# Optimization experiments

Measured on AMD Instinct MI355X. Metric: run time of the kernel, lower is better.

## Reference

```python
import jax, jax.numpy as jnp
import numpy as np

# Complete 32-ary tree of depth 3: vocab = 32**3 = 32768 leaves.
B = 4096       # batch
NHID = 512     # hidden size
BR = 32        # branching factor (num_children at every internal node)
DEPTH = 3      # number of internal-node decisions from root to leaf
V = BR ** DEPTH
NUM_NODES = sum(BR ** k for k in range(DEPTH))  # 1 + 32 + 1024 = 1057

# Static tree-indexing tables (level-order node numbering).
_LEVEL_OFFSET = np.array([sum(BR ** j for j in range(k)) for k in range(DEPTH)], dtype=np.int64)   # [0, 1, 33]
_NODE_DIV = np.array([BR ** (DEPTH - k) for k in range(DEPTH)], dtype=np.int64)                    # node-within-level divisor
_STEP_DIV = np.array([BR ** (DEPTH - 1 - k) for k in range(DEPTH)], dtype=np.int64)                # child-step divisor


def setup_inputs() -> dict:
    key = jax.random.key(0)
    k1, k2, k3 = jax.random.split(key, 3)
    inputs = jax.random.normal(k1, (B, NHID), dtype=jnp.float32)
    labels = jax.random.randint(k2, (B,), 0, V)                     # leaf index per sample
    W = jax.random.normal(k3, (NUM_NODES, NHID, BR), dtype=jnp.float32)  # all node params, stacked
    return {"inputs": inputs, "labels": labels, "W": W}


def reference(inputs, labels, W):
    lab = labels[:, None]                                            # [B, 1]
    node_idx = jnp.asarray(_LEVEL_OFFSET)[None, :] + lab // jnp.asarray(_NODE_DIV)[None, :]  # [B, D] node on path
    steps = (lab // jnp.asarray(_STEP_DIV)[None, :]) % BR            # [B, D] child taken at each node
    Wg = W[node_idx]                                                 # [B, D, NHID, BR] gathered path params
    logits = jnp.einsum('bh,bdhc->bdc', inputs, Wg)                  # [B, D, BR]
    p = jax.nn.softmax(logits, axis=-1)
    step_p = jnp.take_along_axis(p, steps[:, :, None], axis=-1)[..., 0]  # [B, D]
    return jnp.prod(step_p, axis=-1)                                 # [B] path probability
```

## Files before the change

kernel.cpp:

```cpp
#include <hip/hip_runtime.h>


#define NHID  512
#define BR    32
#define BATCH 4096
#define NBUCK 1024
#define SMAX  4
#define GMAX  2048

#define FMA4(A, xv, wv_) do { \
    (A).x = fmaf((xv), (wv_).x, (A).x); \
    (A).y = fmaf((xv), (wv_).y, (A).y); \
    (A).z = fmaf((xv), (wv_).z, (A).z); \
    (A).w = fmaf((xv), (wv_).w, (A).w); } while (0)

__global__ __launch_bounds__(1024) void k_sort(const int* __restrict__ labels,
                                               int* __restrict__ order,
                                               int* __restrict__ ngroups,
                                               int* __restrict__ gdesc) {
    __shared__ int labs[BATCH];
    __shared__ int hist[NBUCK];
    __shared__ int scn[NBUCK];
    __shared__ int gsc[NBUCK];
    const int t = threadIdx.x;

    hist[t] = 0;
    #pragma unroll
    for (int r = 0; r < BATCH / 1024; ++r)
        labs[t + 1024 * r] = labels[t + 1024 * r];
    __syncthreads();
    #pragma unroll
    for (int r = 0; r < BATCH / 1024; ++r)
        atomicAdd(&hist[labs[t + 1024 * r] >> 5], 1);
    __syncthreads();

    const int cnt  = hist[t];
    const int gcnt = (cnt + SMAX - 1) / SMAX;
    scn[t] = cnt;
    gsc[t] = gcnt;
    __syncthreads();
    for (int d = 1; d < NBUCK; d <<= 1) {
        int u1 = (t >= d) ? scn[t - d] : 0;
        int u2 = (t >= d) ? gsc[t - d] : 0;
        __syncthreads();
        scn[t] += u1;
        gsc[t] += u2;
        __syncthreads();
    }
    const int off  = scn[t] - cnt;
    const int goff = gsc[t] - gcnt;
    hist[t] = off;

    for (int j = 0; j < gcnt; ++j)
        gdesc[goff + j] = (off + j * SMAX)
                        | (min(SMAX, cnt - j * SMAX) << 12)
                        | (t << 16);
    if (t == NBUCK - 1) *ngroups = gsc[t];
    __syncthreads();

    #pragma unroll
    for (int r = 0; r < BATCH / 1024; ++r) {
        int j = t + 1024 * r;
        int pos = atomicAdd(&hist[labs[j] >> 5], 1);
        order[pos] = j;
    }
}

__global__ __launch_bounds__(192) void hsm_g4(
    const float* __restrict__ inputs,
    const int* __restrict__ labels,
    const float* __restrict__ W,
    const int* __restrict__ order,
    const int* __restrict__ ngroups,
    const int* __restrict__ gdesc,
    float* __restrict__ out)
{
    __shared__ float xsT[NHID * SMAX];
    __shared__ float pk[3][SMAX];
    __shared__ int   sids[SMAX];
    __shared__ int   slab[SMAX];

    const int gid = blockIdx.x;
    if (gid >= *ngroups) return;
    const int d     = gdesc[gid];
    const int start = d & 0xFFF;
    const int m     = (d >> 12) & 0xF;
    const int g     = d >> 16;
    const int tid   = threadIdx.x;

    if (tid < SMAX) {
        int sid = (tid < m) ? order[start + tid] : -1;
        sids[tid] = sid;
        slab[tid] = (sid >= 0) ? labels[sid] : 0;
    }
    __syncthreads();

    for (int h = tid; h < NHID; h += 192) {
        float v[SMAX];
        #pragma unroll
        for (int s = 0; s < SMAX; ++s) {
            int id = sids[s];
            v[s] = (id >= 0) ? inputs[(size_t)id * NHID + h] : 0.0f;
        }
        ((float4*)xsT)[h] = make_float4(v[0], v[1], v[2], v[3]);
    }
    __syncthreads();

    const int k    = tid >> 6;
    const int lane = tid & 63;
    const int colg = lane & 7;
    const int hsel = lane >> 3;

    const int node = (k == 0) ? 0 : (k == 1) ? 1 + (g >> 5) : 33 + g;
    const int step01 = (k == 0) ? (g >> 5) : (g & 31);

    const float4* wp = (const float4*)(W + (size_t)node * (NHID * BR))
                       + hsel * 8 + colg;
    const float4* xp = (const float4*)xsT + hsel;

    float4 acc[SMAX];
    #pragma unroll
    for (int s = 0; s < SMAX; ++s) acc[s] = make_float4(0, 0, 0, 0);

    #pragma unroll 8
    for (int i = 0; i < 64; ++i) {
        float4 w  = wp[i * 64];
        float4 x4 = xp[i * 8];
        FMA4(acc[0], x4.x, w);
        FMA4(acc[1], x4.y, w);
        FMA4(acc[2], x4.z, w);
        FMA4(acc[3], x4.w, w);
    }

    #pragma unroll
    for (int s = 0; s < SMAX; ++s) {
        #pragma unroll
        for (int mm = 8; mm <= 32; mm <<= 1) {
            acc[s].x += __shfl_xor(acc[s].x, mm);
            acc[s].y += __shfl_xor(acc[s].y, mm);
            acc[s].z += __shfl_xor(acc[s].z, mm);
            acc[s].w += __shfl_xor(acc[s].w, mm);
        }
    }

    #pragma unroll
    for (int s = 0; s < SMAX; ++s) {
        float4 a = acc[s];
        float mx = fmaxf(fmaxf(a.x, a.y), fmaxf(a.z, a.w));
        #pragma unroll
        for (int mm = 1; mm <= 4; mm <<= 1) mx = fmaxf(mx, __shfl_xor(mx, mm));
        float es = expf(a.x - mx) + expf(a.y - mx) + expf(a.z - mx) + expf(a.w - mx);
        #pragma unroll
        for (int mm = 1; mm <= 4; mm <<= 1) es += __shfl_xor(es, mm);

        int step = (k == 2) ? (slab[s] & 31) : step01;
        int e = step & 3;
        float v = (e == 0) ? a.x : (e == 1) ? a.y : (e == 2) ? a.z : a.w;
        float sl = __shfl(v, step >> 2);
        float p = expf(sl - mx) / es;
        if (lane == 0) pk[k][s] = p;
    }
    __syncthreads();

    if (tid < SMAX && sids[tid] >= 0)
        out[sids[tid]] = pk[0][tid] * pk[1][tid] * pk[2][tid];
}

extern "C" void kernel_launch(void* const* d_in, const int* in_sizes, int n_in,
                              void* d_out, int out_size, void* d_ws, size_t ws_size,
                              hipStream_t stream)
{
    const float* inputs = (const float*)d_in[0];
    const int*   labels = (const int*)d_in[1];
    const float* W      = (const float*)d_in[2];
    float* out = (float*)d_out;

    char* ws = (char*)d_ws;
    int* order   = (int*)ws;
    int* ngroups = (int*)(ws + 16384);
    int* gdesc   = (int*)(ws + 16384 + 128);

    k_sort<<<dim3(1),    dim3(1024), 0, stream>>>(labels, order, ngroups, gdesc);
    hsm_g4<<<dim3(GMAX), dim3(192),  0, stream>>>(inputs, labels, W, order,
                                                  ngroups, gdesc, out);
}
```

Baseline: 122.7 us.

## Group up to eight samples per block and use wave-shuffle prefix scan in sort

Raises the number of samples sharing a gathered node weight tile from four to eight, so each W load feeds twice as many FMAs and the number of groups shrinks, with the grid size adjusted to match. The shared-memory Hillis-Steele scan in the sort kernel is replaced by a two-level wavefront shuffle scan to cut barriers. The trade-off is more accumulator registers per thread (32 float accumulators) and more padded empty slots when buckets hold few samples. GMAX of 1536 must cover the worst-case group count, which with about 4 samples per bucket should hold.

```diff
diff --git a/kernel.cpp b/kernel.cpp
--- a/kernel.cpp
+++ b/kernel.cpp
@@ -5,8 +5,8 @@
 #define BR    32
 #define BATCH 4096
 #define NBUCK 1024
-#define SMAX  4
-#define GMAX  2048
+#define SMAX  8
+#define GMAX  1536
 
 #define FMA4(A, xv, wv_) do { \
     (A).x = fmaf((xv), (wv_).x, (A).x); \
@@ -20,9 +20,11 @@
                                                int* __restrict__ gdesc) {
     __shared__ int labs[BATCH];
     __shared__ int hist[NBUCK];
-    __shared__ int scn[NBUCK];
-    __shared__ int gsc[NBUCK];
-    const int t = threadIdx.x;
+    __shared__ int wsum1[16];
+    __shared__ int wsum2[16];
+    const int t  = threadIdx.x;
+    const int wv = t >> 6;
+    const int ln = t & 63;
 
     hist[t] = 0;
     #pragma unroll
@@ -36,27 +38,39 @@
 
     const int cnt  = hist[t];
     const int gcnt = (cnt + SMAX - 1) / SMAX;
-    scn[t] = cnt;
-    gsc[t] = gcnt;
-    __syncthreads();
-    for (int d = 1; d < NBUCK; d <<= 1) {
-        int u1 = (t >= d) ? scn[t - d] : 0;
-        int u2 = (t >= d) ? gsc[t - d] : 0;
-        __syncthreads();
-        scn[t] += u1;
-        gsc[t] += u2;
-        __syncthreads();
-    }
-    const int off  = scn[t] - cnt;
-    const int goff = gsc[t] - gcnt;
+
+    int s1 = cnt, s2 = gcnt;
+    #pragma unroll
+    for (int d = 1; d < 64; d <<= 1) {
+        int u1 = __shfl_up(s1, d);
+        int u2 = __shfl_up(s2, d);
+        if (ln >= d) { s1 += u1; s2 += u2; }
+    }
+    if (ln == 63) { wsum1[wv] = s1; wsum2[wv] = s2; }
+    __syncthreads();
+    if (t < 16) {
+        int a = wsum1[t], b = wsum2[t];
+        #pragma unroll
+        for (int d = 1; d < 16; d <<= 1) {
+            int ua = __shfl_up(a, d, 16);
+            int ub = __shfl_up(b, d, 16);
+            if (t >= d) { a += ua; b += ub; }
+        }
+        wsum1[t] = a; wsum2[t] = b;
+        if (t == 15) *ngroups = b;
+    }
+    __syncthreads();
+    const int base1 = (wv > 0) ? wsum1[wv - 1] : 0;
+    const int base2 = (wv > 0) ? wsum2[wv - 1] : 0;
+    const int off  = base1 + s1 - cnt;
+    const int goff = base2 + s2 - gcnt;
     hist[t] = off;
+    __syncthreads();
 
     for (int j = 0; j < gcnt; ++j)
         gdesc[goff + j] = (off + j * SMAX)
                         | (min(SMAX, cnt - j * SMAX) << 12)
                         | (t << 16);
-    if (t == NBUCK - 1) *ngroups = gsc[t];
-    __syncthreads();
 
     #pragma unroll
     for (int r = 0; r < BATCH / 1024; ++r) {
@@ -66,7 +80,7 @@
     }
 }
 
-__global__ __launch_bounds__(192) void hsm_g4(
+__global__ __launch_bounds__(192) void hsm_g8(
     const float* __restrict__ inputs,
     const int* __restrict__ labels,
     const float* __restrict__ W,
@@ -102,7 +116,9 @@
             int id = sids[s];
             v[s] = (id >= 0) ? inputs[(size_t)id * NHID + h] : 0.0f;
         }
-        ((float4*)xsT)[h] = make_float4(v[0], v[1], v[2], v[3]);
+        float4* dst = (float4*)&xsT[h * SMAX];
+        dst[0] = make_float4(v[0], v[1], v[2], v[3]);
+        dst[1] = make_float4(v[4], v[5], v[6], v[7]);
     }
     __syncthreads();
 
@@ -116,7 +132,7 @@
 
     const float4* wp = (const float4*)(W + (size_t)node * (NHID * BR))
                        + hsel * 8 + colg;
-    const float4* xp = (const float4*)xsT + hsel;
+    const float4* xp = (const float4*)xsT + hsel * 2;
 
     float4 acc[SMAX];
     #pragma unroll
@@ -125,11 +141,12 @@
     #pragma unroll 8
     for (int i = 0; i < 64; ++i) {
         float4 w  = wp[i * 64];
-        float4 x4 = xp[i * 8];
-        FMA4(acc[0], x4.x, w);
-        FMA4(acc[1], x4.y, w);
-        FMA4(acc[2], x4.z, w);
-        FMA4(acc[3], x4.w, w);
+        float4 xa = xp[i * 16];
+        float4 xb = xp[i * 16 + 1];
+        FMA4(acc[0], xa.x, w); FMA4(acc[1], xa.y, w);
+        FMA4(acc[2], xa.z, w); FMA4(acc[3], xa.w, w);
+        FMA4(acc[4], xb.x, w); FMA4(acc[5], xb.y, w);
+        FMA4(acc[6], xb.z, w); FMA4(acc[7], xb.w, w);
     }
 
     #pragma unroll
@@ -181,6 +198,6 @@
     int* gdesc   = (int*)(ws + 16384 + 128);
 
     k_sort<<<dim3(1),    dim3(1024), 0, stream>>>(labels, order, ngroups, gdesc);
-    hsm_g4<<<dim3(GMAX), dim3(192),  0, stream>>>(inputs, labels, W, order,
+    hsm_g8<<<dim3(GMAX), dim3(192),  0, stream>>>(inputs, labels, W, order,
                                                   ngroups, gdesc, out);
 }
```

Measured after the change: 126.2 us. +2.9%, slower.
